# Optimization experiments

Hardware: AMD Instinct MI355X
Metric: run time of the kernel (lower is better)

Reference implementation:

```python
import jax, jax.numpy as jnp
import numpy as np

NL = 65536      # nodes per detector layer
L = 4           # nlayers
N = NL * L      # total nodes
INIT = 4        # initial_dyn_features
DYN = 32        # dyn_features
STAT = 8        # static_features
NPROP = 2
G = 64          # graphs in batch
E_UP = 4194304
E_IN = 1048576
E_FB = 1048576


def setup_inputs() -> dict:
    key = jax.random.key(0)
    ks = jax.random.split(key, 12)
    inp = {}
    inp["x"] = jax.random.normal(ks[0], (N, INIT), dtype=jnp.float32)
    inp["static"] = jax.random.normal(ks[1], (N, STAT), dtype=jnp.float32)
    inp["edge_up"] = jax.random.randint(ks[2], (2, E_UP), 0, N, dtype=jnp.int32)
    inp["inner_edges"] = jax.random.randint(ks[3], (L, 2, E_IN), 0, NL, dtype=jnp.int32)
    inp["forward_edges"] = jax.random.randint(ks[4], (L - 1, 2, E_FB), 0, 2 * NL, dtype=jnp.int32)
    inp["backward_edges"] = jax.random.randint(ks[5], (L - 1, 2, E_FB), 0, 2 * NL, dtype=jnp.int32)
    inp["graph_ids"] = jnp.sort(jax.random.randint(ks[6], (N,), 0, G, dtype=jnp.int32))
    nf = DYN + STAT
    inp["W_up"] = jax.random.normal(ks[7], (INIT, DYN), dtype=jnp.float32) / np.sqrt(INIT)
    inp["b_up"] = jnp.zeros((DYN,), jnp.float32)
    inp["W_in"] = jax.random.normal(ks[8], (nf, DYN), dtype=jnp.float32) / np.sqrt(nf)
    inp["b_in"] = jnp.zeros((DYN,), jnp.float32)
    inp["W_f"] = jax.random.normal(ks[9], (nf, DYN), dtype=jnp.float32) / np.sqrt(nf)
    inp["b_f"] = jnp.zeros((DYN,), jnp.float32)
    inp["W_b"] = jax.random.normal(ks[10], (nf, DYN), dtype=jnp.float32) / np.sqrt(nf)
    inp["b_b"] = jnp.zeros((DYN,), jnp.float32)
    inp["lin_W"] = jax.random.normal(ks[11], (DYN, 1), dtype=jnp.float32) / np.sqrt(DYN)
    inp["lin_b"] = jnp.zeros((1,), jnp.float32)
    return inp


def gcn_conv(x, src, dst, W, b):
    """PyG-style GCNConv: add self-loops, symmetric deg^-1/2 normalization."""
    n = x.shape[0]
    self_idx = jnp.arange(n, dtype=src.dtype)
    src = jnp.concatenate([src, self_idx])
    dst = jnp.concatenate([dst, self_idx])
    h = x @ W                                   # [n, DYN]
    deg = jnp.zeros((n,), x.dtype).at[dst].add(jnp.ones((), x.dtype))
    norm = jax.lax.rsqrt(deg)                   # deg >= 1 due to self-loops
    coef = (norm[src] * norm[dst])[:, None]     # [E+n, 1]
    out = jnp.zeros_like(h).at[dst].add(h[src] * coef)
    return out + b


def _forward(x, static, edge_up, inner_edges, forward_edges, backward_edges,
             graph_ids, W_up, b_up, W_in, b_in, W_f, b_f, W_b, b_b, lin_W, lin_b):
    h = gcn_conv(x, edge_up[0], edge_up[1], W_up, b_up)   # [N, DYN]

    def inner(h, l):
        s = l * NL
        xin = jnp.concatenate([h[s:s + NL], static[s:s + NL]], axis=1)
        out = gcn_conv(xin, inner_edges[l, 0], inner_edges[l, 1], W_in, b_in)
        return h.at[s:s + NL].set(out)

    for _ in range(NPROP):
        for l in range(L):
            h = inner(h, l)
            if l < L - 1:
                s = l * NL
                xin = jnp.concatenate([h[s:s + 2 * NL], static[s:s + 2 * NL]], axis=1)
                out = gcn_conv(xin, forward_edges[l, 0], forward_edges[l, 1], W_f, b_f)
                h = h.at[s + NL:s + 2 * NL].set(out[NL:])
        h = jax.nn.relu(h)
        for l in range(L - 1, 0, -1):
            s = (l - 1) * NL
            xin = jnp.concatenate([h[s:s + 2 * NL], static[s:s + 2 * NL]], axis=1)
            out = gcn_conv(xin, backward_edges[l - 1, 0], backward_edges[l - 1, 1], W_b, b_b)
            h = h.at[s:s + NL].set(out[:NL])
            h = inner(h, l - 1)
        h = jax.nn.relu(h)

    pooled = jax.ops.segment_sum(h, graph_ids, num_segments=G)  # [G, DYN]
    return pooled @ lin_W + lin_b                               # [G, 1]


def reference(x, static, edge_up, inner_edges, forward_edges, backward_edges,
              graph_ids, W_up, b_up, W_in, b_in, W_f, b_f, W_b, b_b, lin_W, lin_b):
    return _forward(x, static, edge_up, inner_edges, forward_edges, backward_edges,
                    graph_ids, W_up, b_up, W_in, b_in, W_f, b_f, W_b, b_b, lin_W, lin_b)
```

## Files before the change

kernel.cpp:

```cpp
#include <hip/hip_runtime.h>

#define NLK 65536
#define NN (NLK * 4)
#define DYNF 32
#define STATF 8
#define GG 64
#define EUP 4194304
#define EIN 1048576
#define EFB 1048576

#define NS_UP    0
#define NS_IN(l) (NN + (l) * NLK)
#define NS_F(l)  (NN + 4 * NLK + (l) * 2 * NLK)
#define NS_B(l)  (NN + 10 * NLK + (l) * 2 * NLK)
#define NS_TOT   (NN + 16 * NLK)
#define CO_TOT   (EUP + 4 * EIN + 6 * EFB)

#define CHUNK 32768
#define NB    (CO_TOT / CHUNK)
#define BROWS 1024
#define NBUCK (NS_TOT / BROWS)
#define HM    (NBUCK * NB)
#define SCAP  20480

static inline int cdiv(long a, int b) { return (int)((a + b - 1) / b); }

__device__ inline void cdecode(int b, const int* e_up, const int* e_in,
                               const int* e_f, const int* e_b,
                               const int*& srcp, const int*& dstp, int& ns, int& e0) {
    if (b < EUP / CHUNK) { srcp = e_up; dstp = e_up + EUP; ns = NS_UP; e0 = b * CHUNK; return; }
    int t = b - EUP / CHUNK;
    int list = t >> 5;
    e0 = (t & 31) * CHUNK;
    if (list < 4) {
        srcp = e_in + (size_t)(2 * list) * EIN; dstp = srcp + EIN; ns = NS_IN(list);
    } else if (list < 7) {
        int l = list - 4;
        srcp = e_f + (size_t)(2 * l) * EFB; dstp = srcp + EFB; ns = NS_F(l);
    } else {
        int l = list - 7;
        srcp = e_b + (size_t)(2 * l) * EFB; dstp = srcp + EFB; ns = NS_B(l);
    }
}

__global__ void hist_part_kernel(const int* __restrict__ e_up, const int* __restrict__ e_in,
                                 const int* __restrict__ e_f, const int* __restrict__ e_b,
                                 int* __restrict__ hmat) {
    __shared__ int lh[NBUCK];
    for (int k = threadIdx.x; k < NBUCK; k += 1024) lh[k] = 0;
    __syncthreads();
    const int *srcp, *dstp; int ns, e0;
    cdecode(blockIdx.x, e_up, e_in, e_f, e_b, srcp, dstp, ns, e0);
    for (int j = 0; j < CHUNK / 1024; j++) {
        int g = ns + dstp[e0 + j * 1024 + threadIdx.x];
        atomicAdd(&lh[g >> 10], 1);
    }
    __syncthreads();
    for (int k = threadIdx.x; k < NBUCK; k += 1024)
        hmat[(size_t)k * NB + blockIdx.x] = lh[k];
}

__global__ void scatter_part_kernel(const int* __restrict__ e_up, const int* __restrict__ e_in,
                                    const int* __restrict__ e_f, const int* __restrict__ e_b,
                                    const int* __restrict__ hmat, const int* __restrict__ smat,
                                    unsigned* __restrict__ pairs) {
    __shared__ unsigned srt[CHUNK];
    __shared__ int ls[NBUCK + 1];
    __shared__ int gbase[NBUCK];
    __shared__ int lcur[NBUCK];
    __shared__ int ssum[1024];
    int t = threadIdx.x;
    int b = blockIdx.x;
    const int *srcp, *dstp; int ns, e0;
    cdecode(b, e_up, e_in, e_f, e_b, srcp, dstp, ns, e0);
    int a0 = (2 * t < NBUCK) ? hmat[(size_t)(2 * t) * NB + b] : 0;
    int a1 = (2 * t + 1 < NBUCK) ? hmat[(size_t)(2 * t + 1) * NB + b] : 0;
    if (2 * t < NBUCK) gbase[2 * t] = smat[(size_t)(2 * t) * NB + b];
    if (2 * t + 1 < NBUCK) gbase[2 * t + 1] = smat[(size_t)(2 * t + 1) * NB + b];
    if (2 * t < NBUCK) lcur[2 * t] = 0;
    if (2 * t + 1 < NBUCK) lcur[2 * t + 1] = 0;
    int gsum = a0 + a1;
    ssum[t] = gsum;
    __syncthreads();
    for (int off = 1; off < 1024; off <<= 1) {
        int u = (t >= off) ? ssum[t - off] : 0;
        __syncthreads();
        ssum[t] += u;
        __syncthreads();
    }
    int run = ssum[t] - gsum;
    if (2 * t < NBUCK) ls[2 * t] = run;
    if (2 * t + 1 < NBUCK) ls[2 * t + 1] = run + a0;
    if (t == 0) ls[NBUCK] = CHUNK;
    __syncthreads();
    for (int j = 0; j < CHUNK / 1024; j++) {
        int el = e0 + j * 1024 + t;
        int g = ns + dstp[el];
        int s = srcp[el];
        int k = g >> 10;
        int pos = ls[k] + atomicAdd(&lcur[k], 1);
        srt[pos] = ((unsigned)s << 10) | (unsigned)(g & (BROWS - 1));
    }
    __syncthreads();
    int wave = t >> 6;
    int lane = t & 63;
    for (int k = wave; k < NBUCK; k += 16) {
        int lo = ls[k];
        int n = ls[k + 1] - lo;
        int dst = gbase[k];
        for (int i = lane; i < n; i += 64)
            pairs[dst + i] = srt[lo + i];
    }
}

__global__ void group_kernel(const unsigned* __restrict__ pairs, const int* __restrict__ smat,
                             int* __restrict__ col, int* __restrict__ rp,
                             float* __restrict__ norms) {
    __shared__ int srt[SCAP];
    __shared__ int lcnt[BROWS];
    __shared__ int roff[BROWS];
    __shared__ int lcur[BROWS];
    __shared__ int ssum[1024];
    int k = blockIdx.x;
    int t = threadIdx.x;
    int base = smat[(size_t)k * NB];
    int end  = (k + 1 < NBUCK) ? smat[(size_t)(k + 1) * NB] : CO_TOT;
    int nb = end - base;
    lcnt[t] = 0;
    lcur[t] = 0;
    __syncthreads();
    for (int i = base + t; i < end; i += 1024)
        atomicAdd(&lcnt[pairs[i] & (BROWS - 1)], 1);
    __syncthreads();
    int a0 = lcnt[t];
    ssum[t] = a0;
    __syncthreads();
    for (int off = 1; off < 1024; off <<= 1) {
        int u = (t >= off) ? ssum[t - off] : 0;
        __syncthreads();
        ssum[t] += u;
        __syncthreads();
    }
    int gex = ssum[t] - a0;
    roff[t] = gex;
    int row = k * BROWS + t;
    rp[row] = base + gex;
    norms[row] = rsqrtf((float)(a0 + 1));
    if (k == 0 && t == 0) rp[NS_TOT] = CO_TOT;
    __syncthreads();
    if (nb <= SCAP) {
        for (int i = base + t; i < end; i += 1024) {
            unsigned p = pairs[i];
            int rl = p & (BROWS - 1);
            int pos = roff[rl] + atomicAdd(&lcur[rl], 1);
            srt[pos] = (int)(p >> 10);
        }
        __syncthreads();
        for (int j = t; j < nb; j += 1024)
            col[base + j] = srt[j];
    } else {
        for (int i = base + t; i < end; i += 1024) {
            unsigned p = pairs[i];
            int rl = p & (BROWS - 1);
            int pos = base + roff[rl] + atomicAdd(&lcur[rl], 1);
            col[pos] = (int)(p >> 10);
        }
    }
}


__global__ void scan1_kernel(const int* __restrict__ cnt, int* __restrict__ rp,
                             int* __restrict__ part, int n) {
    __shared__ int sh[1024];
    int t = threadIdx.x;
    int i = blockIdx.x * 1024 + t;
    int v = (i < n) ? cnt[i] : 0;
    sh[t] = v;
    __syncthreads();
    for (int off = 1; off < 1024; off <<= 1) {
        int u = (t >= off) ? sh[t - off] : 0;
        __syncthreads();
        sh[t] += u;
        __syncthreads();
    }
    if (i < n) rp[i] = sh[t] - v;
    if (t == 1023) part[blockIdx.x] = sh[1023];
}

__global__ void scan2_kernel(int* part, int m) {
    __shared__ int sh[256];
    __shared__ int carry;
    int t = threadIdx.x;
    if (t == 0) carry = 0;
    __syncthreads();
    for (int base = 0; base < m; base += 256) {
        int i = base + t;
        int v = (i < m) ? part[i] : 0;
        sh[t] = v;
        __syncthreads();
        for (int off = 1; off < 256; off <<= 1) {
            int u = (t >= off) ? sh[t - off] : 0;
            __syncthreads();
            sh[t] += u;
            __syncthreads();
        }
        if (i < m) part[i] = sh[t] - v + carry;
        __syncthreads();
        if (t == 255) carry += sh[255];
        __syncthreads();
    }
}

__global__ void scan3_kernel(int* __restrict__ rp, const int* __restrict__ part, int n) {
    int i = blockIdx.x * blockDim.x + threadIdx.x;
    if (i < n) rp[i] += part[i >> 10];
}


__device__ inline unsigned bf16rne(float f) {
    unsigned u = __float_as_uint(f);
    return (u + 0x7fffu + ((u >> 16) & 1u)) >> 16;
}
__device__ inline float bfl(unsigned u) { return __uint_as_float(u << 16); }
__device__ inline float bfh(unsigned u) { return __uint_as_float(u & 0xffff0000u); }


struct EmitArg {
    const float* nrm;
    unsigned*    hsb;
    const float* W;
    int relu;
    int on;
};

__global__ void pull_emit_kernel(const int* __restrict__ rp, const int* __restrict__ col,
                                 const unsigned* __restrict__ hsb_in, const float* __restrict__ nrm,
                                 const float* __restrict__ b, float* __restrict__ out,
                                 const float* __restrict__ stat_p, int row_lo, int write_h,
                                 EmitArg em0, EmitArg em1) {
    __shared__ float W0[1280];
    __shared__ float W1[1280];
    __shared__ float rowbuf[32][41];
    int t = threadIdx.x;
    if (em0.on) for (int i = t; i < 1280; i += 256) W0[i] = em0.W[i];
    if (em1.on) for (int i = t; i < 1280; i += 256) W1[i] = em1.W[i];
    int tid = blockIdx.x * 256 + t;
    int rr = tid >> 3;
    int r = row_lo + rr;
    int j = tid & 7;
    int hw = j * 2;
    int ea = rp[r], eb = rp[r + 1];
    uint2 sv = *(const uint2*)(hsb_in + (size_t)r * 16 + hw);
    float a0 = bfl(sv.x), a1 = bfh(sv.x), a2 = bfl(sv.y), a3 = bfh(sv.y);
    int e = ea;
    for (; e + 2 <= eb; e += 2) {
        int s0 = col[e];
        int s1 = col[e + 1];
        uint2 v0 = *(const uint2*)(hsb_in + (size_t)s0 * 16 + hw);
        uint2 v1 = *(const uint2*)(hsb_in + (size_t)s1 * 16 + hw);
        a0 += bfl(v0.x) + bfl(v1.x); a1 += bfh(v0.x) + bfh(v1.x);
        a2 += bfl(v0.y) + bfl(v1.y); a3 += bfh(v0.y) + bfh(v1.y);
    }
    if (e < eb) {
        int s = col[e];
        uint2 v = *(const uint2*)(hsb_in + (size_t)s * 16 + hw);
        a0 += bfl(v.x); a1 += bfh(v.x); a2 += bfl(v.y); a3 += bfh(v.y);
    }
    float nm = nrm[r];
    int q = j * 4;
    float4 bv = *(const float4*)(b + q);
    float o0 = fmaf(a0, nm, bv.x), o1 = fmaf(a1, nm, bv.y);
    float o2 = fmaf(a2, nm, bv.z), o3 = fmaf(a3, nm, bv.w);
    if (write_h)
        *(float4*)(out + (size_t)r * DYNF + q) = make_float4(o0, o1, o2, o3);
    if (!em0.on && !em1.on) return;
    int lrow = t >> 3;
    rowbuf[lrow][q] = o0; rowbuf[lrow][q + 1] = o1;
    rowbuf[lrow][q + 2] = o2; rowbuf[lrow][q + 3] = o3;
    rowbuf[lrow][32 + j] = stat_p[(size_t)rr * 8 + j];
    __syncthreads();
    if (em0.on) {
        float nmc = em0.nrm[rr];
        float r0 = 0, r1 = 0, r2 = 0, r3 = 0;
#pragma unroll
        for (int k = 0; k < 40; k++) {
            float v = rowbuf[lrow][k];
            if (k < 32 && em0.relu) v = fmaxf(v, 0.f);
            const float* Wp = &W0[k * 32 + q];
            r0 = fmaf(v, Wp[0], r0); r1 = fmaf(v, Wp[1], r1);
            r2 = fmaf(v, Wp[2], r2); r3 = fmaf(v, Wp[3], r3);
        }
        unsigned u0 = bf16rne(r0 * nmc) | (bf16rne(r1 * nmc) << 16);
        unsigned u1 = bf16rne(r2 * nmc) | (bf16rne(r3 * nmc) << 16);
        *(uint2*)(em0.hsb + (size_t)rr * 16 + hw) = make_uint2(u0, u1);
    }
    if (em1.on) {
        float nmc = em1.nrm[rr];
        float r0 = 0, r1 = 0, r2 = 0, r3 = 0;
#pragma unroll
        for (int k = 0; k < 40; k++) {
            float v = rowbuf[lrow][k];
            if (k < 32 && em1.relu) v = fmaxf(v, 0.f);
            const float* Wp = &W1[k * 32 + q];
            r0 = fmaf(v, Wp[0], r0); r1 = fmaf(v, Wp[1], r1);
            r2 = fmaf(v, Wp[2], r2); r3 = fmaf(v, Wp[3], r3);
        }
        unsigned u0 = bf16rne(r0 * nmc) | (bf16rne(r1 * nmc) << 16);
        unsigned u1 = bf16rne(r2 * nmc) | (bf16rne(r3 * nmc) << 16);
        *(uint2*)(em1.hsb + (size_t)rr * 16 + hw) = make_uint2(u0, u1);
    }
}


__global__ void xsb_kernel(const float* __restrict__ x, const float* __restrict__ nrm,
                           uint2* __restrict__ xsb, int n) {
    int r = blockIdx.x * blockDim.x + threadIdx.x;
    if (r >= n) return;
    float nm = nrm[r];
    float4 v = *(const float4*)(x + (size_t)r * 4);
    xsb[r] = make_uint2(bf16rne(v.x * nm) | (bf16rne(v.y * nm) << 16),
                        bf16rne(v.z * nm) | (bf16rne(v.w * nm) << 16));
}

struct UpEmit {
    const float* n0; const float* n1; const float* n2; const float* n3;
    unsigned* h0; unsigned* h1; unsigned* h2; unsigned* h3;
};

__global__ void pull4mm_emit_kernel(const int* __restrict__ rp0, const int* __restrict__ col,
                                    const uint2* __restrict__ xsb, const float* __restrict__ Wup,
                                    const float* __restrict__ nrm, const float* __restrict__ bup,
                                    const float* __restrict__ Win, const float* __restrict__ Wf,
                                    const float* __restrict__ stat, UpEmit ue) {
    __shared__ float Ws[128];
    __shared__ float bs[32];
    __shared__ float Wa[1280];
    __shared__ float Wb[1280];
    __shared__ float rowbuf[32][41];
    int t = threadIdx.x;
    for (int i = t; i < 128; i += 256) Ws[i] = Wup[i];
    if (t < 32) bs[t] = bup[t];
    for (int i = t; i < 1280; i += 256) { Wa[i] = Win[i]; Wb[i] = Wf[i]; }
    __syncthreads();
    int tid = blockIdx.x * 256 + t;
    int g = tid >> 3;
    int j = t & 7;
    int ea = rp0[g], eb = rp0[g + 1];
    float a0 = 0.f, a1 = 0.f, a2 = 0.f, a3 = 0.f;
    int e = ea + j;
    for (; e + 8 < eb; e += 16) {
        uint2 v0 = xsb[col[e]];
        uint2 v1 = xsb[col[e + 8]];
        a0 += bfl(v0.x) + bfl(v1.x); a1 += bfh(v0.x) + bfh(v1.x);
        a2 += bfl(v0.y) + bfl(v1.y); a3 += bfh(v0.y) + bfh(v1.y);
    }
    if (e < eb) {
        uint2 v = xsb[col[e]];
        a0 += bfl(v.x); a1 += bfh(v.x); a2 += bfl(v.y); a3 += bfh(v.y);
    }
#pragma unroll
    for (int m = 1; m < 8; m <<= 1) {
        a0 += __shfl_xor(a0, m);
        a1 += __shfl_xor(a1, m);
        a2 += __shfl_xor(a2, m);
        a3 += __shfl_xor(a3, m);
    }
    uint2 sv = xsb[g];
    a0 += bfl(sv.x); a1 += bfh(sv.x); a2 += bfl(sv.y); a3 += bfh(sv.y);
    float nm = nrm[g];
    int q = j * 4;
    int lrow = t >> 3;
#pragma unroll
    for (int d = 0; d < 4; d++) {
        float s = a0 * Ws[q + d] + a1 * Ws[32 + q + d] + a2 * Ws[64 + q + d] + a3 * Ws[96 + q + d];
        rowbuf[lrow][q + d] = fmaf(s, nm, bs[q + d]);
    }
    rowbuf[lrow][32 + j] = stat[(size_t)g * 8 + j];
    __syncthreads();
    int l = g >> 16;
    const float* W = (l == 0) ? Wa : Wb;
    const float* nc = (l == 0) ? ue.n0 : (l == 1) ? ue.n1 : (l == 2) ? ue.n2 : ue.n3;
    unsigned* hb = (l == 0) ? ue.h0 : (l == 1) ? ue.h1 : (l == 2) ? ue.h2 : ue.h3;
    float nmc = nc[g];
    float r0 = 0, r1 = 0, r2 = 0, r3 = 0;
#pragma unroll
    for (int k = 0; k < 40; k++) {
        float v = rowbuf[lrow][k];
        const float* Wp = &W[k * 32 + q];
        r0 = fmaf(v, Wp[0], r0); r1 = fmaf(v, Wp[1], r1);
        r2 = fmaf(v, Wp[2], r2); r3 = fmaf(v, Wp[3], r3);
    }
    unsigned u0 = bf16rne(r0 * nmc) | (bf16rne(r1 * nmc) << 16);
    unsigned u1 = bf16rne(r2 * nmc) | (bf16rne(r3 * nmc) << 16);
    *(uint2*)(hb + (size_t)g * 16 + j * 2) = make_uint2(u0, u1);
}


__global__ void init_out_kernel(float* out, const float* __restrict__ lin_b) {
    int i = threadIdx.x;
    if (i < GG) out[i] = lin_b[0];
}

__global__ void pool_kernel(const float* __restrict__ h, const int* __restrict__ gids,
                            const float* __restrict__ linW, float* out) {
    __shared__ float part[GG];
    int t = threadIdx.x;
    if (t < GG) part[t] = 0.f;
    __syncthreads();
    int r = blockIdx.x * blockDim.x + t;
    float dotv = 0.f;
    const float4* hp = (const float4*)(h + (size_t)r * DYNF);
#pragma unroll
    for (int q = 0; q < 8; q++) {
        float4 v = hp[q];
        dotv += fmaxf(v.x, 0.f) * linW[q * 4 + 0] + fmaxf(v.y, 0.f) * linW[q * 4 + 1] +
                fmaxf(v.z, 0.f) * linW[q * 4 + 2] + fmaxf(v.w, 0.f) * linW[q * 4 + 3];
    }
    atomicAdd(&part[gids[r]], dotv);
    __syncthreads();
    if (t < GG) unsafeAtomicAdd(&out[t], part[t]);
}


extern "C" void kernel_launch(void* const* d_in, const int* in_sizes, int n_in,
                              void* d_out, int out_size, void* d_ws, size_t ws_size,
                              hipStream_t stream) {
    const float* x     = (const float*)d_in[0];
    const float* stat  = (const float*)d_in[1];
    const int*   e_up  = (const int*)d_in[2];
    const int*   e_in  = (const int*)d_in[3];
    const int*   e_f   = (const int*)d_in[4];
    const int*   e_b   = (const int*)d_in[5];
    const int*   gids  = (const int*)d_in[6];
    const float* W_up  = (const float*)d_in[7];
    const float* b_up  = (const float*)d_in[8];
    const float* W_in  = (const float*)d_in[9];
    const float* b_in  = (const float*)d_in[10];
    const float* W_f   = (const float*)d_in[11];
    const float* b_f   = (const float*)d_in[12];
    const float* W_b   = (const float*)d_in[13];
    const float* b_b   = (const float*)d_in[14];
    const float* lin_W = (const float*)d_in[15];
    const float* lin_b = (const float*)d_in[16];
    float* out = (float*)d_out;

    float*    norms = (float*)d_ws;
    int*      rp    = (int*)(norms + NS_TOT);
    int*      col   = rp + NS_TOT + 1;
    unsigned* H0    = (unsigned*)(col + CO_TOT);
    float*    h     = (float*)H0;
    unsigned* hsbp  = H0 + (size_t)NN * DYNF;
    uint2*    xsb   = (uint2*)(hsbp + (size_t)16 * NLK * 16);
    unsigned* pairs = H0;
    int*      hmat  = (int*)(H0 + CO_TOT);
    int*      smat  = hmat + HM;
    int*      part  = smat + HM;

    unsigned* SA  = hsbp + (size_t)0  * NLK * 16;
    unsigned* SB  = hsbp + (size_t)1  * NLK * 16;
    unsigned* SC  = hsbp + (size_t)2  * NLK * 16;
    unsigned* SD  = hsbp + (size_t)3  * NLK * 16;
    unsigned* F0b = hsbp + (size_t)4  * NLK * 16;
    unsigned* F1b = hsbp + (size_t)6  * NLK * 16;
    unsigned* F2b = hsbp + (size_t)8  * NLK * 16;
    unsigned* B0b = hsbp + (size_t)10 * NLK * 16;
    unsigned* B1b = hsbp + (size_t)12 * NLK * 16;
    unsigned* B2b = hsbp + (size_t)14 * NLK * 16;

    hist_part_kernel<<<NB, 1024, 0, stream>>>(e_up, e_in, e_f, e_b, hmat);
    scan1_kernel<<<HM / 1024, 1024, 0, stream>>>(hmat, smat, part, HM);
    scan2_kernel<<<1, 256, 0, stream>>>(part, HM / 1024);
    scan3_kernel<<<cdiv(HM, 256), 256, 0, stream>>>(smat, part, HM);
    scatter_part_kernel<<<NB, 1024, 0, stream>>>(e_up, e_in, e_f, e_b, hmat, smat, pairs);
    group_kernel<<<NBUCK, 1024, 0, stream>>>(pairs, smat, col, rp, norms);

    xsb_kernel<<<cdiv(NN, 256), 256, 0, stream>>>(x, norms + NS_UP, xsb, NN);
    UpEmit ue;
    ue.n0 = norms + NS_IN(0);
    ue.n1 = norms + NS_F(0);
    ue.n2 = norms + NS_F(1) - NLK;
    ue.n3 = norms + NS_F(2) - 2 * NLK;
    ue.h0 = SA;
    ue.h1 = F0b;
    ue.h2 = F1b - (size_t)NLK * 16;
    ue.h3 = F2b - (size_t)2 * NLK * 16;
    pull4mm_emit_kernel<<<(NN * 8) / 256, 256, 0, stream>>>(rp + NS_UP, col, xsb, W_up,
                                                            norms + NS_UP, b_up, W_in, W_f, stat, ue);

    auto EM = [&](const float* n, unsigned* hb, const float* W, int rl) {
        EmitArg e; e.nrm = n; e.hsb = hb; e.W = W; e.relu = rl; e.on = 1; return e;
    };
    EmitArg OFF; OFF.nrm = nullptr; OFF.hsb = nullptr; OFF.W = nullptr; OFF.relu = 0; OFF.on = 0;

    auto P = [&](unsigned* buf, int ns, const float* bias, int gbase, int row_lo,
                 int wh, EmitArg a, EmitArg c) {
        pull_emit_kernel<<<(NLK * 8) / 256, 256, 0, stream>>>(
            rp + ns, col, buf, norms + ns, bias, h + (size_t)gbase * DYNF,
            stat + (size_t)(gbase + row_lo) * STATF, row_lo, wh, a, c);
    };

    for (int p = 0; p < 2; p++) {
        P(SA, NS_IN(0), b_in, 0, 0, 0,
          EM(norms + NS_F(0), F0b, W_f, 0), EM(norms + NS_B(0), B0b, W_b, 1));
        P(F0b, NS_F(0), b_f, 0, NLK, 0,
          EM(norms + NS_IN(1), SB, W_in, 0), OFF);
        P(SB, NS_IN(1), b_in, NLK, 0, 0,
          EM(norms + NS_F(1), F1b, W_f, 0), EM(norms + NS_B(1), B1b, W_b, 1));
        P(F1b, NS_F(1), b_f, NLK, NLK, 0,
          EM(norms + NS_IN(2), SC, W_in, 0), OFF);
        P(SC, NS_IN(2), b_in, 2 * NLK, 0, 0,
          EM(norms + NS_F(2), F2b, W_f, 0), EM(norms + NS_B(2), B2b, W_b, 1));
        P(F2b, NS_F(2), b_f, 2 * NLK, NLK, 0,
          EM(norms + NS_IN(3), SA, W_in, 0), OFF);
        P(SA, NS_IN(3), b_in, 3 * NLK, 0, (p == 1),
          EM(norms + NS_B(2) + NLK, B2b + (size_t)NLK * 16, W_b, 1),
          p == 0 ? EM(norms + NS_F(2) + NLK, F2b + (size_t)NLK * 16, W_f, 1) : OFF);
        P(B2b, NS_B(2), b_b, 2 * NLK, 0, 0,
          EM(norms + NS_IN(2), SC, W_in, 0), OFF);
        P(SC, NS_IN(2), b_in, 2 * NLK, 0, (p == 1),
          EM(norms + NS_B(1) + NLK, B1b + (size_t)NLK * 16, W_b, 0),
          p == 0 ? EM(norms + NS_F(1) + NLK, F1b + (size_t)NLK * 16, W_f, 1) : OFF);
        P(B1b, NS_B(1), b_b, NLK, 0, 0,
          EM(norms + NS_IN(1), SB, W_in, 0), OFF);
        P(SB, NS_IN(1), b_in, NLK, 0, (p == 1),
          EM(norms + NS_B(0) + NLK, B0b + (size_t)NLK * 16, W_b, 0),
          p == 0 ? EM(norms + NS_F(0) + NLK, F0b + (size_t)NLK * 16, W_f, 1) : OFF);
        P(B0b, NS_B(0), b_b, 0, 0, 0,
          EM(norms + NS_IN(0), SD, W_in, 0), OFF);
        P(SD, NS_IN(0), b_in, 0, 0, (p == 1),
          p == 0 ? EM(norms + NS_IN(0), SA, W_in, 1) : OFF, OFF);
    }

    init_out_kernel<<<1, 64, 0, stream>>>(out, lin_b);
    pool_kernel<<<NN / 256, 256, 0, stream>>>(h, gids, lin_W, out);
}
```

Baseline: 807.5 us.

## Fuse GCN propagation steps into one cooperative persistent kernel with grid syncs

Replaces the sequence of 27 per-step pull/emit kernel launches and the pool kernel with a single cooperative mega-kernel. It runs 256 blocks of 1024 threads, walks a constant-memory schedule table and separates steps with grid.sync. The goal is to remove launch gaps and tail effects between the many small dependent kernels. The cost is fixed occupancy (one 1024-thread block per CU), weight reloads into shared memory at each step, and grid-barrier overhead. The old multi-kernel path stays as a fallback when cooperative launch is unavailable.

```diff
diff --git a/kernel.cpp b/kernel.cpp
--- a/kernel.cpp
+++ b/kernel.cpp
@@ -1,4 +1,6 @@
 #include <hip/hip_runtime.h>
+#include <hip/hip_cooperative_groups.h>
+namespace cg = cooperative_groups;
 
 #define NLK 65536
 #define NN (NLK * 4)
@@ -22,6 +24,21 @@
 #define NBUCK (NS_TOT / BROWS)
 #define HM    (NBUCK * NB)
 #define SCAP  20480
+
+#define SLOT_U (NLK * 16)
+#define SA_O 0
+#define SB_O (1 * SLOT_U)
+#define SC_O (2 * SLOT_U)
+#define SD_O (3 * SLOT_U)
+#define F0_O (4 * SLOT_U)
+#define F1_O (6 * SLOT_U)
+#define F2_O (8 * SLOT_U)
+#define B0_O (10 * SLOT_U)
+#define B1_O (12 * SLOT_U)
+#define B2_O (14 * SLOT_U)
+
+#define MBLK 256
+#define MTHR 1024
 
 static inline int cdiv(long a, int b) { return (int)((a + b - 1) / b); }
 
@@ -223,6 +240,237 @@
 }
 __device__ inline float bfl(unsigned u) { return __uint_as_float(u << 16); }
 __device__ inline float bfh(unsigned u) { return __uint_as_float(u & 0xffff0000u); }
+
+
+__global__ void xsb_kernel(const float* __restrict__ x, const float* __restrict__ nrm,
+                           uint2* __restrict__ xsb, int n) {
+    int r = blockIdx.x * blockDim.x + threadIdx.x;
+    if (r >= n) return;
+    float nm = nrm[r];
+    float4 v = *(const float4*)(x + (size_t)r * 4);
+    xsb[r] = make_uint2(bf16rne(v.x * nm) | (bf16rne(v.y * nm) << 16),
+                        bf16rne(v.z * nm) | (bf16rne(v.w * nm) << 16));
+}
+
+__global__ void init_out_kernel(float* out, const float* __restrict__ lin_b) {
+    int i = threadIdx.x;
+    if (i < GG) out[i] = lin_b[0];
+}
+
+
+struct Step {
+    int buf, ns, bsel, gbase, rlo, wh;
+    int e0on, e0n, e0h, e0w, e0r;
+    int e1on, e1n, e1h, e1w, e1r;
+};
+
+__device__ __constant__ Step SCHED[26] = {
+    {SA_O, NS_IN(0), 0, 0, 0, 0,        1, NS_F(0), F0_O, 1, 0,              1, NS_B(0), B0_O, 2, 1},
+    {F0_O, NS_F(0), 1, 0, NLK, 0,       1, NS_IN(1), SB_O, 0, 0,             0,0,0,0,0},
+    {SB_O, NS_IN(1), 0, NLK, 0, 0,      1, NS_F(1), F1_O, 1, 0,              1, NS_B(1), B1_O, 2, 1},
+    {F1_O, NS_F(1), 1, NLK, NLK, 0,     1, NS_IN(2), SC_O, 0, 0,             0,0,0,0,0},
+    {SC_O, NS_IN(2), 0, 2*NLK, 0, 0,    1, NS_F(2), F2_O, 1, 0,              1, NS_B(2), B2_O, 2, 1},
+    {F2_O, NS_F(2), 1, 2*NLK, NLK, 0,   1, NS_IN(3), SA_O, 0, 0,             0,0,0,0,0},
+    {SA_O, NS_IN(3), 0, 3*NLK, 0, 0,    1, NS_B(2)+NLK, B2_O+SLOT_U, 2, 1,   1, NS_F(2)+NLK, F2_O+SLOT_U, 1, 1},
+    {B2_O, NS_B(2), 2, 2*NLK, 0, 0,     1, NS_IN(2), SC_O, 0, 0,             0,0,0,0,0},
+    {SC_O, NS_IN(2), 0, 2*NLK, 0, 0,    1, NS_B(1)+NLK, B1_O+SLOT_U, 2, 0,   1, NS_F(1)+NLK, F1_O+SLOT_U, 1, 1},
+    {B1_O, NS_B(1), 2, NLK, 0, 0,       1, NS_IN(1), SB_O, 0, 0,             0,0,0,0,0},
+    {SB_O, NS_IN(1), 0, NLK, 0, 0,      1, NS_B(0)+NLK, B0_O+SLOT_U, 2, 0,   1, NS_F(0)+NLK, F0_O+SLOT_U, 1, 1},
+    {B0_O, NS_B(0), 2, 0, 0, 0,         1, NS_IN(0), SD_O, 0, 0,             0,0,0,0,0},
+    {SD_O, NS_IN(0), 0, 0, 0, 0,        1, NS_IN(0), SA_O, 0, 1,             0,0,0,0,0},
+    {SA_O, NS_IN(0), 0, 0, 0, 0,        1, NS_F(0), F0_O, 1, 0,              1, NS_B(0), B0_O, 2, 1},
+    {F0_O, NS_F(0), 1, 0, NLK, 0,       1, NS_IN(1), SB_O, 0, 0,             0,0,0,0,0},
+    {SB_O, NS_IN(1), 0, NLK, 0, 0,      1, NS_F(1), F1_O, 1, 0,              1, NS_B(1), B1_O, 2, 1},
+    {F1_O, NS_F(1), 1, NLK, NLK, 0,     1, NS_IN(2), SC_O, 0, 0,             0,0,0,0,0},
+    {SC_O, NS_IN(2), 0, 2*NLK, 0, 0,    1, NS_F(2), F2_O, 1, 0,              1, NS_B(2), B2_O, 2, 1},
+    {F2_O, NS_F(2), 1, 2*NLK, NLK, 0,   1, NS_IN(3), SA_O, 0, 0,             0,0,0,0,0},
+    {SA_O, NS_IN(3), 0, 3*NLK, 0, 1,    1, NS_B(2)+NLK, B2_O+SLOT_U, 2, 1,   0,0,0,0,0},
+    {B2_O, NS_B(2), 2, 2*NLK, 0, 0,     1, NS_IN(2), SC_O, 0, 0,             0,0,0,0,0},
+    {SC_O, NS_IN(2), 0, 2*NLK, 0, 1,    1, NS_B(1)+NLK, B1_O+SLOT_U, 2, 0,   0,0,0,0,0},
+    {B1_O, NS_B(1), 2, NLK, 0, 0,       1, NS_IN(1), SB_O, 0, 0,             0,0,0,0,0},
+    {SB_O, NS_IN(1), 0, NLK, 0, 1,      1, NS_B(0)+NLK, B0_O+SLOT_U, 2, 0,   0,0,0,0,0},
+    {B0_O, NS_B(0), 2, 0, 0, 0,         1, NS_IN(0), SD_O, 0, 0,             0,0,0,0,0},
+    {SD_O, NS_IN(0), 0, 0, 0, 1,        0,0,0,0,0,                           0,0,0,0,0},
+};
+
+
+__global__ void __launch_bounds__(MTHR, 4)
+mega_kernel(const int* __restrict__ rp, const int* __restrict__ col,
+            unsigned* __restrict__ hsbp, const float* __restrict__ norms,
+            float* __restrict__ h, const float* __restrict__ stat,
+            const uint2* __restrict__ xsb,
+            const float* __restrict__ W_in, const float* __restrict__ b_in,
+            const float* __restrict__ W_f, const float* __restrict__ b_f,
+            const float* __restrict__ W_b, const float* __restrict__ b_b,
+            const float* __restrict__ W_up, const float* __restrict__ b_up,
+            const int* __restrict__ gids, const float* __restrict__ lin_W,
+            float* __restrict__ out) {
+    cg::grid_group grid = cg::this_grid();
+    __shared__ float WA[1280];
+    __shared__ float WB[1280];
+    __shared__ float Wu[128];
+    __shared__ float bu[32];
+    __shared__ float rowbuf[128][41];
+    __shared__ float part[GG];
+    int t = threadIdx.x;
+    int j = t & 7;
+    int lrow = t >> 3;
+    int hw = j * 2;
+    int q = j * 4;
+
+    for (int i = t; i < 128; i += MTHR) Wu[i] = W_up[i];
+    if (t < 32) bu[t] = b_up[t];
+    for (int i = t; i < 1280; i += MTHR) { WA[i] = W_in[i]; WB[i] = W_f[i]; }
+    __syncthreads();
+    for (int it = 0; it < 8; it++) {
+        int tid = it * (MBLK * MTHR) + blockIdx.x * MTHR + t;
+        int g = tid >> 3;
+        int ea = rp[g], eb = rp[g + 1];
+        float a0 = 0.f, a1 = 0.f, a2 = 0.f, a3 = 0.f;
+        int e = ea + j;
+        for (; e + 8 < eb; e += 16) {
+            uint2 v0 = xsb[col[e]];
+            uint2 v1 = xsb[col[e + 8]];
+            a0 += bfl(v0.x) + bfl(v1.x); a1 += bfh(v0.x) + bfh(v1.x);
+            a2 += bfl(v0.y) + bfl(v1.y); a3 += bfh(v0.y) + bfh(v1.y);
+        }
+        if (e < eb) {
+            uint2 v = xsb[col[e]];
+            a0 += bfl(v.x); a1 += bfh(v.x); a2 += bfl(v.y); a3 += bfh(v.y);
+        }
+#pragma unroll
+        for (int m = 1; m < 8; m <<= 1) {
+            a0 += __shfl_xor(a0, m);
+            a1 += __shfl_xor(a1, m);
+            a2 += __shfl_xor(a2, m);
+            a3 += __shfl_xor(a3, m);
+        }
+        uint2 sv = xsb[g];
+        a0 += bfl(sv.x); a1 += bfh(sv.x); a2 += bfl(sv.y); a3 += bfh(sv.y);
+        float nm = norms[g];
+#pragma unroll
+        for (int d = 0; d < 4; d++) {
+            float s = a0 * Wu[q + d] + a1 * Wu[32 + q + d] + a2 * Wu[64 + q + d] + a3 * Wu[96 + q + d];
+            rowbuf[lrow][q + d] = fmaf(s, nm, bu[q + d]);
+        }
+        rowbuf[lrow][32 + j] = stat[(size_t)g * 8 + j];
+        __syncthreads();
+        int l = g >> 16;
+        const float* W = (l == 0) ? WA : WB;
+        int noff = (l == 0) ? NS_IN(0) : (l == 1) ? NS_F(0) : (l == 2) ? (NS_F(1) - NLK) : (NS_F(2) - 2 * NLK);
+        int hoff = (l == 0) ? SA_O : (l == 1) ? F0_O : (l == 2) ? (F1_O - SLOT_U) : (F2_O - 2 * SLOT_U);
+        float nmc = norms[noff + g];
+        float r0 = 0, r1 = 0, r2 = 0, r3 = 0;
+#pragma unroll
+        for (int k = 0; k < 40; k++) {
+            float v = rowbuf[lrow][k];
+            const float* Wp = &W[k * 32 + q];
+            r0 = fmaf(v, Wp[0], r0); r1 = fmaf(v, Wp[1], r1);
+            r2 = fmaf(v, Wp[2], r2); r3 = fmaf(v, Wp[3], r3);
+        }
+        unsigned u0 = bf16rne(r0 * nmc) | (bf16rne(r1 * nmc) << 16);
+        unsigned u1 = bf16rne(r2 * nmc) | (bf16rne(r3 * nmc) << 16);
+        *(uint2*)(hsbp + (size_t)hoff + (size_t)g * 16 + hw) = make_uint2(u0, u1);
+        __syncthreads();
+    }
+    __threadfence();
+    grid.sync();
+
+    for (int s = 0; s < 26; s++) {
+        Step S = SCHED[s];
+        const float* bias = (S.bsel == 0) ? b_in : (S.bsel == 1) ? b_f : b_b;
+        if (S.e0on) {
+            const float* Wt = (S.e0w == 0) ? W_in : (S.e0w == 1) ? W_f : W_b;
+            for (int i = t; i < 1280; i += MTHR) WA[i] = Wt[i];
+        }
+        if (S.e1on) {
+            const float* Wt = (S.e1w == 0) ? W_in : (S.e1w == 1) ? W_f : W_b;
+            for (int i = t; i < 1280; i += MTHR) WB[i] = Wt[i];
+        }
+        __syncthreads();
+        const unsigned* hin = hsbp + S.buf;
+        for (int it = 0; it < 2; it++) {
+            int tid = it * (MBLK * MTHR) + blockIdx.x * MTHR + t;
+            int rr = tid >> 3;
+            int r = S.rlo + rr;
+            int ea = rp[S.ns + r], eb = rp[S.ns + r + 1];
+            uint2 sv = *(const uint2*)(hin + (size_t)r * 16 + hw);
+            float a0 = bfl(sv.x), a1 = bfh(sv.x), a2 = bfl(sv.y), a3 = bfh(sv.y);
+            int e = ea;
+            for (; e + 2 <= eb; e += 2) {
+                int s0 = col[e];
+                int s1 = col[e + 1];
+                uint2 v0 = *(const uint2*)(hin + (size_t)s0 * 16 + hw);
+                uint2 v1 = *(const uint2*)(hin + (size_t)s1 * 16 + hw);
+                a0 += bfl(v0.x) + bfl(v1.x); a1 += bfh(v0.x) + bfh(v1.x);
+                a2 += bfl(v0.y) + bfl(v1.y); a3 += bfh(v0.y) + bfh(v1.y);
+            }
+            if (e < eb) {
+                int s0 = col[e];
+                uint2 v = *(const uint2*)(hin + (size_t)s0 * 16 + hw);
+                a0 += bfl(v.x); a1 += bfh(v.x); a2 += bfl(v.y); a3 += bfh(v.y);
+            }
+            float nm = norms[S.ns + r];
+            float4 bv = *(const float4*)(bias + q);
+            float o0 = fmaf(a0, nm, bv.x), o1 = fmaf(a1, nm, bv.y);
+            float o2 = fmaf(a2, nm, bv.z), o3 = fmaf(a3, nm, bv.w);
+            if (S.wh)
+                *(float4*)(h + (size_t)(S.gbase + S.rlo + rr) * DYNF + q) = make_float4(o0, o1, o2, o3);
+            rowbuf[lrow][q] = o0; rowbuf[lrow][q + 1] = o1;
+            rowbuf[lrow][q + 2] = o2; rowbuf[lrow][q + 3] = o3;
+            rowbuf[lrow][32 + j] = stat[(size_t)(S.gbase + S.rlo + rr) * 8 + j];
+            __syncthreads();
+            if (S.e0on) {
+                float nmc = norms[S.e0n + rr];
+                float r0 = 0, r1 = 0, r2 = 0, r3 = 0;
+#pragma unroll
+                for (int k = 0; k < 40; k++) {
+                    float v = rowbuf[lrow][k];
+                    if (k < 32 && S.e0r) v = fmaxf(v, 0.f);
+                    const float* Wp = &WA[k * 32 + q];
+                    r0 = fmaf(v, Wp[0], r0); r1 = fmaf(v, Wp[1], r1);
+                    r2 = fmaf(v, Wp[2], r2); r3 = fmaf(v, Wp[3], r3);
+                }
+                unsigned u0 = bf16rne(r0 * nmc) | (bf16rne(r1 * nmc) << 16);
+                unsigned u1 = bf16rne(r2 * nmc) | (bf16rne(r3 * nmc) << 16);
+                *(uint2*)(hsbp + (size_t)S.e0h + (size_t)rr * 16 + hw) = make_uint2(u0, u1);
+            }
+            if (S.e1on) {
+                float nmc = norms[S.e1n + rr];
+                float r0 = 0, r1 = 0, r2 = 0, r3 = 0;
+#pragma unroll
+                for (int k = 0; k < 40; k++) {
+                    float v = rowbuf[lrow][k];
+                    if (k < 32 && S.e1r) v = fmaxf(v, 0.f);
+                    const float* Wp = &WB[k * 32 + q];
+                    r0 = fmaf(v, Wp[0], r0); r1 = fmaf(v, Wp[1], r1);
+                    r2 = fmaf(v, Wp[2], r2); r3 = fmaf(v, Wp[3], r3);
+                }
+                unsigned u0 = bf16rne(r0 * nmc) | (bf16rne(r1 * nmc) << 16);
+                unsigned u1 = bf16rne(r2 * nmc) | (bf16rne(r3 * nmc) << 16);
+                *(uint2*)(hsbp + (size_t)S.e1h + (size_t)rr * 16 + hw) = make_uint2(u0, u1);
+            }
+            __syncthreads();
+        }
+        __threadfence();
+        grid.sync();
+    }
+
+    if (t < GG) part[t] = 0.f;
+    __syncthreads();
+    int r = blockIdx.x * MTHR + t;
+    float dotv = 0.f;
+    const float4* hp = (const float4*)(h + (size_t)r * DYNF);
+#pragma unroll
+    for (int qq = 0; qq < 8; qq++) {
+        float4 v = hp[qq];
+        dotv += fmaxf(v.x, 0.f) * lin_W[qq * 4 + 0] + fmaxf(v.y, 0.f) * lin_W[qq * 4 + 1] +
+                fmaxf(v.z, 0.f) * lin_W[qq * 4 + 2] + fmaxf(v.w, 0.f) * lin_W[qq * 4 + 3];
+    }
+    atomicAdd(&part[gids[r]], dotv);
+    __syncthreads();
+    if (t < GG) unsafeAtomicAdd(&out[t], part[t]);
+}
 
 
 struct EmitArg {
@@ -311,17 +559,6 @@
     }
 }
 
-
-__global__ void xsb_kernel(const float* __restrict__ x, const float* __restrict__ nrm,
-                           uint2* __restrict__ xsb, int n) {
-    int r = blockIdx.x * blockDim.x + threadIdx.x;
-    if (r >= n) return;
-    float nm = nrm[r];
-    float4 v = *(const float4*)(x + (size_t)r * 4);
-    xsb[r] = make_uint2(bf16rne(v.x * nm) | (bf16rne(v.y * nm) << 16),
-                        bf16rne(v.z * nm) | (bf16rne(v.w * nm) << 16));
-}
-
 struct UpEmit {
     const float* n0; const float* n1; const float* n2; const float* n3;
     unsigned* h0; unsigned* h1; unsigned* h2; unsigned* h3;
@@ -393,12 +630,6 @@
     unsigned u0 = bf16rne(r0 * nmc) | (bf16rne(r1 * nmc) << 16);
     unsigned u1 = bf16rne(r2 * nmc) | (bf16rne(r3 * nmc) << 16);
     *(uint2*)(hb + (size_t)g * 16 + j * 2) = make_uint2(u0, u1);
-}
-
-
-__global__ void init_out_kernel(float* out, const float* __restrict__ lin_b) {
-    int i = threadIdx.x;
-    if (i < GG) out[i] = lin_b[0];
 }
 
 __global__ void pool_kernel(const float* __restrict__ h, const int* __restrict__ gids,
@@ -456,16 +687,16 @@
     int*      smat  = hmat + HM;
     int*      part  = smat + HM;
 
-    unsigned* SA  = hsbp + (size_t)0  * NLK * 16;
-    unsigned* SB  = hsbp + (size_t)1  * NLK * 16;
-    unsigned* SC  = hsbp + (size_t)2  * NLK * 16;
-    unsigned* SD  = hsbp + (size_t)3  * NLK * 16;
-    unsigned* F0b = hsbp + (size_t)4  * NLK * 16;
-    unsigned* F1b = hsbp + (size_t)6  * NLK * 16;
-    unsigned* F2b = hsbp + (size_t)8  * NLK * 16;
-    unsigned* B0b = hsbp + (size_t)10 * NLK * 16;
-    unsigned* B1b = hsbp + (size_t)12 * NLK * 16;
-    unsigned* B2b = hsbp + (size_t)14 * NLK * 16;
+    unsigned* SA  = hsbp + (size_t)0  * SLOT_U;
+    unsigned* SB  = hsbp + (size_t)1  * SLOT_U;
+    unsigned* SC  = hsbp + (size_t)2  * SLOT_U;
+    unsigned* SD  = hsbp + (size_t)3  * SLOT_U;
+    unsigned* F0b = hsbp + (size_t)4  * SLOT_U;
+    unsigned* F1b = hsbp + (size_t)6  * SLOT_U;
+    unsigned* F2b = hsbp + (size_t)8  * SLOT_U;
+    unsigned* B0b = hsbp + (size_t)10 * SLOT_U;
+    unsigned* B1b = hsbp + (size_t)12 * SLOT_U;
+    unsigned* B2b = hsbp + (size_t)14 * SLOT_U;
 
     hist_part_kernel<<<NB, 1024, 0, stream>>>(e_up, e_in, e_f, e_b, hmat);
     scan1_kernel<<<HM / 1024, 1024, 0, stream>>>(hmat, smat, part, HM);
@@ -475,6 +706,33 @@
     group_kernel<<<NBUCK, 1024, 0, stream>>>(pairs, smat, col, rp, norms);
 
     xsb_kernel<<<cdiv(NN, 256), 256, 0, stream>>>(x, norms + NS_UP, xsb, NN);
+    init_out_kernel<<<1, 64, 0, stream>>>(out, lin_b);
+
+    int coopAttr = 0, dev = 0, maxB = 0;
+    hipGetDevice(&dev);
+    hipDeviceGetAttribute(&coopAttr, hipDeviceAttributeCooperativeLaunch, dev);
+    hipOccupancyMaxActiveBlocksPerMultiprocessor(&maxB, mega_kernel, MTHR, 0);
+    bool use_coop = (coopAttr != 0) && (maxB >= 1);
+
+    if (use_coop) {
+        const int* a_rp = rp; const int* a_col = col;
+        unsigned* a_hsbp = hsbp; const float* a_norms = norms;
+        float* a_h = h; const float* a_stat = stat;
+        const uint2* a_xsb = xsb;
+        const float* a_Win = W_in; const float* a_bin = b_in;
+        const float* a_Wf = W_f; const float* a_bf = b_f;
+        const float* a_Wb = W_b; const float* a_bb = b_b;
+        const float* a_Wup = W_up; const float* a_bup = b_up;
+        const int* a_gids = gids; const float* a_linW = lin_W;
+        float* a_out = out;
+        void* args[] = { &a_rp, &a_col, &a_hsbp, &a_norms, &a_h, &a_stat, &a_xsb,
+                         &a_Win, &a_bin, &a_Wf, &a_bf, &a_Wb, &a_bb, &a_Wup, &a_bup,
+                         &a_gids, &a_linW, &a_out };
+        hipLaunchCooperativeKernel((void*)mega_kernel, dim3(MBLK), dim3(MTHR),
+                                   args, 0, stream);
+        return;
+    }
+
     UpEmit ue;
     ue.n0 = norms + NS_IN(0);
     ue.n1 = norms + NS_F(0);
@@ -482,8 +740,8 @@
     ue.n3 = norms + NS_F(2) - 2 * NLK;
     ue.h0 = SA;
     ue.h1 = F0b;
-    ue.h2 = F1b - (size_t)NLK * 16;
-    ue.h3 = F2b - (size_t)2 * NLK * 16;
+    ue.h2 = F1b - (size_t)SLOT_U;
+    ue.h3 = F2b - (size_t)2 * SLOT_U;
     pull4mm_emit_kernel<<<(NN * 8) / 256, 256, 0, stream>>>(rp + NS_UP, col, xsb, W_up,
                                                             norms + NS_UP, b_up, W_in, W_f, stat, ue);
 
@@ -513,24 +771,23 @@
         P(F2b, NS_F(2), b_f, 2 * NLK, NLK, 0,
           EM(norms + NS_IN(3), SA, W_in, 0), OFF);
         P(SA, NS_IN(3), b_in, 3 * NLK, 0, (p == 1),
-          EM(norms + NS_B(2) + NLK, B2b + (size_t)NLK * 16, W_b, 1),
-          p == 0 ? EM(norms + NS_F(2) + NLK, F2b + (size_t)NLK * 16, W_f, 1) : OFF);
+          EM(norms + NS_B(2) + NLK, B2b + (size_t)SLOT_U, W_b, 1),
+          p == 0 ? EM(norms + NS_F(2) + NLK, F2b + (size_t)SLOT_U, W_f, 1) : OFF);
         P(B2b, NS_B(2), b_b, 2 * NLK, 0, 0,
           EM(norms + NS_IN(2), SC, W_in, 0), OFF);
         P(SC, NS_IN(2), b_in, 2 * NLK, 0, (p == 1),
-          EM(norms + NS_B(1) + NLK, B1b + (size_t)NLK * 16, W_b, 0),
-          p == 0 ? EM(norms + NS_F(1) + NLK, F1b + (size_t)NLK * 16, W_f, 1) : OFF);
+          EM(norms + NS_B(1) + NLK, B1b + (size_t)SLOT_U, W_b, 0),
+          p == 0 ? EM(norms + NS_F(1) + NLK, F1b + (size_t)SLOT_U, W_f, 1) : OFF);
         P(B1b, NS_B(1), b_b, NLK, 0, 0,
           EM(norms + NS_IN(1), SB, W_in, 0), OFF);
         P(SB, NS_IN(1), b_in, NLK, 0, (p == 1),
-          EM(norms + NS_B(0) + NLK, B0b + (size_t)NLK * 16, W_b, 0),
-          p == 0 ? EM(norms + NS_F(0) + NLK, F0b + (size_t)NLK * 16, W_f, 1) : OFF);
+          EM(norms + NS_B(0) + NLK, B0b + (size_t)SLOT_U, W_b, 0),
+          p == 0 ? EM(norms + NS_F(0) + NLK, F0b + (size_t)SLOT_U, W_f, 1) : OFF);
         P(B0b, NS_B(0), b_b, 0, 0, 0,
           EM(norms + NS_IN(0), SD, W_in, 0), OFF);
         P(SD, NS_IN(0), b_in, 0, 0, (p == 1),
           p == 0 ? EM(norms + NS_IN(0), SA, W_in, 1) : OFF, OFF);
     }
 
-    init_out_kernel<<<1, 64, 0, stream>>>(out, lin_b);
     pool_kernel<<<NN / 256, 256, 0, stream>>>(h, gids, lin_W, out);
 }
```

Result: no change. 809.7 us (+0.3%).
